# Kernel tuning notes

Hardware: AMD Instinct MI355X
Metric: run time of the kernel (lower is better)

Reference implementation:

```python
import jax, jax.numpy as jnp
import numpy as np

B, K, D, H = 4, 2048, 768, 12
HD = D // H
NEG = -1e30  # stands in for -inf in the additive mask


def setup_inputs() -> dict:
    key = jax.random.key(0)
    ks = jax.random.split(key, 11)
    s = 1.0 / np.sqrt(D)
    inp = {
        "x": jax.random.normal(ks[0], (B, K, D), jnp.float32),
        "is_context": jax.random.randint(ks[1], (B, K), 0, 2) > 0,
        "Wq": jax.random.normal(ks[2], (D, D), jnp.float32) * s,
        "bq": jax.random.normal(ks[3], (D,), jnp.float32) * 0.01,
        "Wk": jax.random.normal(ks[4], (D, D), jnp.float32) * s,
        "bk": jax.random.normal(ks[5], (D,), jnp.float32) * 0.01,
        "Wv": jax.random.normal(ks[6], (D, D), jnp.float32) * s,
        "bv": jax.random.normal(ks[7], (D,), jnp.float32) * 0.01,
        "Wo": jax.random.normal(ks[8], (D, D), jnp.float32) * s,
        "bo": jax.random.normal(ks[9], (D,), jnp.float32) * 0.01,
    }
    return inp


def reference(x, is_context, Wq, bq, Wk, bk, Wv, bv, Wo, bo):
    b, k_len, d = x.shape
    scale = 1.0 / jnp.sqrt(jnp.asarray(HD, x.dtype))
    # torch nn.Linear: y = x @ W.T + b
    q = (x @ Wq.T + bq).reshape(b, k_len, H, HD).transpose(0, 2, 1, 3)  # [B,H,K,hd]
    kk = (x @ Wk.T + bk).reshape(b, k_len, H, HD).transpose(0, 2, 1, 3)
    v = (x @ Wv.T + bv).reshape(b, k_len, H, HD).transpose(0, 2, 1, 3)

    ctx = is_context  # [B,K] bool
    # allowed[b,i,j]: context rows attend only to context cols; target rows attend to all
    allowed = (ctx[:, :, None] & ctx[:, None, :]) | (~ctx)[:, :, None]  # [B,K,K]

    scores = jnp.einsum("bhqd,bhkd->bhqk", q, kk) * scale  # [B,H,K,K]
    scores = jnp.where(allowed[:, None, :, :], scores, NEG)
    attn = jax.nn.softmax(scores, axis=-1)
    out = jnp.einsum("bhqk,bhkd->bhqd", attn, v)  # [B,H,K,hd]
    out = out.transpose(0, 2, 1, 3).reshape(b, k_len, d)
    return out @ Wo.T + bo
```

## Files before the change

### kernel.cpp

```cpp
#include <hip/hip_runtime.h>
#include <hip/hip_bf16.h>

constexpr int BATCH = 4;
constexpr int SEQ   = 2048;
constexpr int DIM   = 768;
constexpr int NH    = 12;
constexpr int HDIM  = 64;

typedef __attribute__((ext_vector_type(8))) short bf16x8;
typedef __attribute__((ext_vector_type(4))) float f32x4;
typedef __attribute__((ext_vector_type(4))) short s16x4;

__device__ inline short f2bf(float f) {
    union { float f; unsigned u; } v; v.f = f;
    unsigned r = (v.u + 0x7fff + ((v.u >> 16) & 1)) >> 16;
    return (short)r;
}

__device__ inline unsigned pack_bf16x2(float a, float b) {
    union { __hip_bfloat162 h; unsigned u; } c;
    c.h = __float22bfloat162_rn(make_float2(a, b));
    return c.u;
}

__device__ inline float fast_exp2(float x) {
#if __has_builtin(__builtin_amdgcn_exp2f)
    return __builtin_amdgcn_exp2f(x);
#else
    return __expf(x * 0.6931471805599453f);
#endif
}

__device__ inline void gld16(const short* g, short* l) {
    __builtin_amdgcn_global_load_lds(
        (const __attribute__((address_space(1))) void*)g,
        (__attribute__((address_space(3))) void*)l, 16, 0, 0);
}

__device__ inline bool ctx_at(const void* p, bool isU8, int idx) {
    return isU8 ? (((const unsigned char*)p)[idx] != 0)
                : (((const int*)p)[idx] != 0);
}

__global__ __launch_bounds__(256) void prep_kernel(
    const float* __restrict__ x,  const float* __restrict__ Wq,
    const float* __restrict__ Wk, const float* __restrict__ Wv,
    const float* __restrict__ Wo,
    short* __restrict__ xb,  short* __restrict__ Wqb,
    short* __restrict__ Wkb, short* __restrict__ Wvb,
    short* __restrict__ Wob,
    const unsigned char* __restrict__ ctxm, int ctxbytes, int* __restrict__ flag) {
    const int blk = blockIdx.x;
    constexpr int XBLK = (BATCH * SEQ * DIM / 4) / 256;
    constexpr int WBLK = (DIM * DIM / 4) / 256;

    if (blk == XBLK + 4 * WBLK) {
        __shared__ int cnt;
        if (threadIdx.x == 0) cnt = 0;
        __syncthreads();
        int local = 0;
        for (int i = threadIdx.x; i < ctxbytes; i += 256)
            if ((i & 3) != 0 && ctxm[i] != 0) local++;
        atomicAdd(&cnt, local);
        __syncthreads();
        if (threadIdx.x == 0) *flag = (cnt > 0) ? 1 : 0;
        return;
    }

    const float* src; short* dst; int i;
    if (blk < XBLK) {
        src = x; dst = xb;
        i = blk * 256 + threadIdx.x;
    } else {
        const int r = blk - XBLK;
        const int w = r / WBLK;
        src = (w == 0) ? Wq : (w == 1) ? Wk : (w == 2) ? Wv : Wo;
        dst = (w == 0) ? Wqb : (w == 1) ? Wkb : (w == 2) ? Wvb : Wob;
        i = (r - w * WBLK) * 256 + threadIdx.x;
    }
    float4 v = ((const float4*)src)[i];
    s16x4 o;
    o.x = f2bf(v.x); o.y = f2bf(v.y); o.z = f2bf(v.z); o.w = f2bf(v.w);
    ((s16x4*)dst)[i] = o;
}

template <bool BF16OUT>
__global__ __launch_bounds__(256) void gemm_mfma(
    const short* __restrict__ A,
    const short* __restrict__ W0, const float* __restrict__ bias0, void* __restrict__ C0,
    const short* __restrict__ W1, const float* __restrict__ bias1, void* __restrict__ C1,
    const short* __restrict__ W2, const float* __restrict__ bias2, void* __restrict__ C2,
    float scale0) {
    constexpr int N  = DIM;
    constexpr int Kd = DIM;

    const short* W; const float* bias; void* C; float scale;
    if (blockIdx.z == 0)      { W = W0; bias = bias0; C = C0; scale = scale0; }
    else if (blockIdx.z == 1) { W = W1; bias = bias1; C = C1; scale = 1.f; }
    else                      { W = W2; bias = bias2; C = C2; scale = 1.f; }

    const int tid  = threadIdx.x;
    const int wave = tid >> 6;
    const int lane = tid & 63;
    const int quad = lane >> 4;
    const int l16  = lane & 15;
    const int wm   = wave & 1;
    const int wn   = wave >> 1;
    const int m0   = blockIdx.y * 128;
    const int n0   = blockIdx.x * 128;

    __shared__ short As[128 * 32];
    __shared__ short Bs[128 * 32];

    const int srow = tid >> 2;
    const int skq  = tid & 3;
    const short* Ag = A + (size_t)(m0 + srow) * Kd + skq * 8;
    const short* Wg = W + (size_t)(n0 + srow) * Kd + skq * 8;
    short* AsP = As + srow * 32 + skq * 8;
    short* BsP = Bs + srow * 32 + skq * 8;

    f32x4 acc[4][4] = {};

    for (int kt = 0; kt < Kd; kt += 32) {
        __syncthreads();
        gld16(Ag + kt,                AsP);
        gld16(Ag + kt + 64 * Kd,      AsP + 64 * 32);
        gld16(Wg + kt,                BsP);
        gld16(Wg + kt + 64 * Kd,      BsP + 64 * 32);
        __syncthreads();

        bf16x8 af[4], bfr[4];
#pragma unroll
        for (int mt = 0; mt < 4; ++mt)
            af[mt] = *(const bf16x8*)&As[(wm * 64 + mt * 16 + l16) * 32 + quad * 8];
#pragma unroll
        for (int nt = 0; nt < 4; ++nt)
            bfr[nt] = *(const bf16x8*)&Bs[(wn * 64 + nt * 16 + l16) * 32 + quad * 8];
#pragma unroll
        for (int mt = 0; mt < 4; ++mt)
#pragma unroll
            for (int nt = 0; nt < 4; ++nt)
                acc[mt][nt] = __builtin_amdgcn_mfma_f32_16x16x32_bf16(
                    af[mt], bfr[nt], acc[mt][nt], 0, 0, 0);
    }

    float bv[4];
#pragma unroll
    for (int nt = 0; nt < 4; ++nt) bv[nt] = bias[n0 + wn * 64 + nt * 16 + l16];

#pragma unroll
    for (int mt = 0; mt < 4; ++mt)
#pragma unroll
        for (int nt = 0; nt < 4; ++nt)
#pragma unroll
            for (int reg = 0; reg < 4; ++reg) {
                const int m = m0 + wm * 64 + mt * 16 + quad * 4 + reg;
                const int n = n0 + wn * 64 + nt * 16 + l16;
                const float v = (acc[mt][nt][reg] + bv[nt]) * scale;
                if (BF16OUT) ((short*)C)[(size_t)m * N + n] = f2bf(v);
                else         ((float*)C)[(size_t)m * N + n] = v;
            }
}

__global__ __launch_bounds__(256) void vtrans_kernel(
    const short* __restrict__ Vb, short* __restrict__ Vtg) {
    const int b  = blockIdx.z;
    const int h  = blockIdx.y;
    const int k0 = blockIdx.x * 64;
    const int pw = threadIdx.x & 15;
    const int d0 = (threadIdx.x >> 4) * 4;

    const int ks = pw >> 3;
    const int w  = pw & 7;
    const int q  = w >> 1;
    const int kbase = ks * 32 + ((w & 1) ? (16 + (q ^ 2) * 4) : (q * 4));

    s16x4 vr[4];
#pragma unroll
    for (int g = 0; g < 4; ++g)
        vr[g] = *(const s16x4*)(Vb + (size_t)(b * SEQ + k0 + kbase + g) * DIM
                                + h * HDIM + d0);
#pragma unroll
    for (int i = 0; i < 4; ++i) {
        s16x4 o = {vr[0][i], vr[1][i], vr[2][i], vr[3][i]};
        *(s16x4*)(Vtg + (size_t)((b * NH + h) * HDIM + d0 + i) * SEQ + k0 + 4 * pw) = o;
    }
}

__global__ __launch_bounds__(256, 3) void attn_mfma8(
    const short* __restrict__ Qb, const short* __restrict__ Kb,
    const short* __restrict__ Vtg, const void* __restrict__ ctxp,
    const int* __restrict__ flagp, short* __restrict__ Ob) {
    const int swz  = (blockIdx.x & 7) * 96 + (blockIdx.x >> 3);
    const int qc   = swz & 15;
    const int h    = (swz >> 4) % NH;
    const int b    = swz / (16 * NH);
    const int q0   = qc * 128;
    const int tid  = threadIdx.x;
    const int wave = tid >> 6;
    const int lane = tid & 63;
    const int quad = lane >> 4;
    const int l16  = lane & 15;
    const bool isU8 = (*flagp != 0);

    __shared__ short Ks[3][64 * 64];
    __shared__ short Vs[3][64 * 64];

    const short* Kg = Kb + (size_t)b * SEQ * DIM + h * HDIM;
    const short* Vg = Vtg + (size_t)(b * NH + h) * HDIM * SEQ;

    const int r0 = tid >> 3;
    const int j0 = (tid & 7) ^ (r0 & 7);
    const int sw = l16 & 7;

    bf16x8 qf[2][2];
#pragma unroll
    for (int rg = 0; rg < 2; ++rg) {
        const short* qp = Qb + (size_t)(b * SEQ + q0 + wave * 32 + rg * 16 + l16) * DIM
                        + h * HDIM + quad * 8;
        qf[rg][0] = *(const bf16x8*)qp;
        qf[rg][1] = *(const bf16x8*)(qp + 32);
    }

    unsigned nmb[2];
#pragma unroll
    for (int rg = 0; rg < 2; ++rg)
        nmb[rg] = ctx_at(ctxp, isU8,
            b * SEQ + q0 + wave * 32 + rg * 16 + l16) ? 0u : 0xFFFFFFFFu;

    constexpr int NT = SEQ / 64;
    unsigned kbits = 0;
    for (int t = 0; t < NT; ++t)
        kbits |= (ctx_at(ctxp, isU8, b * SEQ + t * 64 + lane) ? 1u : 0u) << t;

    bf16x8 ones;
#pragma unroll
    for (int i = 0; i < 8; ++i) ones[i] = (short)0x3F80;

    f32x4 accl[2] = {};
    f32x4 acc[2][4] = {};

    auto stage = [&](int t) {
        short* KD = Ks[t % 3];
        short* VD = Vs[t % 3];
        const int kn = t * 64;
        gld16(Kg + (size_t)(kn + r0) * DIM + j0 * 8,      KD + tid * 8);
        gld16(Kg + (size_t)(kn + r0 + 32) * DIM + j0 * 8, KD + (tid + 256) * 8);
        gld16(Vg + (size_t)r0 * SEQ + kn + j0 * 8,        VD + tid * 8);
        gld16(Vg + (size_t)(r0 + 32) * SEQ + kn + j0 * 8, VD + (tid + 256) * 8);
    };

    stage(0);
    stage(1);

    for (int t = 0; t < NT; ++t) {
        const short* BK = Ks[t % 3];
        const short* BV = Vs[t % 3];

        __builtin_amdgcn_s_barrier();
        __builtin_amdgcn_sched_barrier(0);
        if (t + 2 < NT) stage(t + 2);

        if (t < NT - 2)       asm volatile("s_waitcnt vmcnt(8)" ::: "memory");
        else if (t == NT - 2) asm volatile("s_waitcnt vmcnt(4)" ::: "memory");
        else                  asm volatile("s_waitcnt vmcnt(0)" ::: "memory");
        __builtin_amdgcn_sched_barrier(0);
        __builtin_amdgcn_s_barrier();
        __builtin_amdgcn_sched_barrier(0);

        const unsigned long long kmask = __ballot((kbits >> t) & 1u);

        f32x4 s4[4][2] = {};
        __builtin_amdgcn_s_setprio(1);
#pragma unroll
        for (int ks = 0; ks < 2; ++ks) {
            bf16x8 kf[4];
#pragma unroll
            for (int g = 0; g < 4; ++g)
                kf[g] = *(const bf16x8*)
                    &BK[(g * 16 + l16) * 64 + (((ks * 4 + quad) ^ sw)) * 8];
#pragma unroll
            for (int g = 0; g < 4; ++g) {
                s4[g][0] = __builtin_amdgcn_mfma_f32_16x16x32_bf16(kf[g], qf[0][ks], s4[g][0], 0, 0, 0);
                s4[g][1] = __builtin_amdgcn_mfma_f32_16x16x32_bf16(kf[g], qf[1][ks], s4[g][1], 0, 0, 0);
            }
        }
        __builtin_amdgcn_s_setprio(0);

        unsigned mw[2][4];
#pragma unroll
        for (int ks = 0; ks < 2; ++ks)
#pragma unroll
            for (int w = 0; w < 4; ++w) {
                const int base = 32 * ks + ((w >> 1) & 1) * 16 + quad * 4 + (w & 1) * 2;
                const unsigned two = (unsigned)(kmask >> base) & 3u;
                mw[ks][w] = ((two & 1u) ? 0x0000FFFFu : 0u) |
                            ((two & 2u) ? 0xFFFF0000u : 0u);
            }

        bf16x8 pa[2][2];
#pragma unroll
        for (int rg = 0; rg < 2; ++rg) {
            const unsigned nm = nmb[rg];
#pragma unroll
            for (int ks = 0; ks < 2; ++ks) {
                const int g0 = 2 * ks, g1 = 2 * ks + 1;
                const float e0 = fast_exp2(s4[g0][rg][0]);
                const float e1 = fast_exp2(s4[g0][rg][1]);
                const float e2 = fast_exp2(s4[g0][rg][2]);
                const float e3 = fast_exp2(s4[g0][rg][3]);
                const float e4 = fast_exp2(s4[g1][rg][0]);
                const float e5 = fast_exp2(s4[g1][rg][1]);
                const float e6 = fast_exp2(s4[g1][rg][2]);
                const float e7 = fast_exp2(s4[g1][rg][3]);
                const unsigned wA0 = pack_bf16x2(e0, e1) & (nm | mw[ks][0]);
                const unsigned wA1 = pack_bf16x2(e2, e3) & (nm | mw[ks][1]);
                const unsigned wB0 = pack_bf16x2(e4, e5) & (nm | mw[ks][2]);
                const unsigned wB1 = pack_bf16x2(e6, e7) & (nm | mw[ks][3]);
                const unsigned pB0 = (unsigned)__shfl((int)wB0, lane ^ 32);
                const unsigned pB1 = (unsigned)__shfl((int)wB1, lane ^ 32);
                union { bf16x8 v; unsigned u[4]; } tb;
                tb.u[0] = wA0; tb.u[1] = wA1; tb.u[2] = pB0; tb.u[3] = pB1;
                pa[rg][ks] = tb.v;
            }
        }

        __builtin_amdgcn_s_setprio(1);
#pragma unroll
        for (int ks = 0; ks < 2; ++ks) {
            accl[0] = __builtin_amdgcn_mfma_f32_16x16x32_bf16(pa[0][ks], ones, accl[0], 0, 0, 0);
            accl[1] = __builtin_amdgcn_mfma_f32_16x16x32_bf16(pa[1][ks], ones, accl[1], 0, 0, 0);
#pragma unroll
            for (int dt = 0; dt < 4; ++dt) {
                bf16x8 vf = *(const bf16x8*)
                    &BV[(dt * 16 + l16) * 64 + (((ks * 4 + quad) ^ sw)) * 8];
                acc[0][dt] = __builtin_amdgcn_mfma_f32_16x16x32_bf16(pa[0][ks], vf, acc[0][dt], 0, 0, 0);
                acc[1][dt] = __builtin_amdgcn_mfma_f32_16x16x32_bf16(pa[1][ks], vf, acc[1][dt], 0, 0, 0);
            }
        }
        __builtin_amdgcn_s_setprio(0);
    }

    float inv[2][4];
#pragma unroll
    for (int rg = 0; rg < 2; ++rg)
#pragma unroll
        for (int reg = 0; reg < 4; ++reg)
            inv[rg][reg] = 1.f / accl[rg][reg];

#pragma unroll
    for (int rg = 0; rg < 2; ++rg)
#pragma unroll
        for (int dt = 0; dt < 4; ++dt)
#pragma unroll
            for (int reg = 0; reg < 4; ++reg) {
                const int q = q0 + wave * 32 + rg * 16 + quad * 4 + reg;
                Ob[(size_t)(b * SEQ + q) * DIM + h * HDIM + dt * 16 + l16] =
                    f2bf(acc[rg][dt][reg] * inv[rg][reg]);
            }
}

extern "C" void kernel_launch(void* const* d_in, const int* in_sizes, int n_in,
                              void* d_out, int out_size, void* d_ws, size_t ws_size,
                              hipStream_t stream) {
    const float* x   = (const float*)d_in[0];
    const void*  ctx = d_in[1];
    const float* Wq  = (const float*)d_in[2];
    const float* bq  = (const float*)d_in[3];
    const float* Wk  = (const float*)d_in[4];
    const float* bk  = (const float*)d_in[5];
    const float* Wv  = (const float*)d_in[6];
    const float* bv  = (const float*)d_in[7];
    const float* Wo  = (const float*)d_in[8];
    const float* bo  = (const float*)d_in[9];
    float* out = (float*)d_out;

    char* ws = (char*)d_ws;
    int* flag = (int*)ws;
    const size_t bufbf = (size_t)BATCH * SEQ * DIM * sizeof(short);
    const size_t wbuf  = (size_t)DIM * DIM * sizeof(short);
    short* xb  = (short*)(ws + 256);
    short* Qb  = (short*)(ws + 256 + bufbf);
    short* Kb  = (short*)(ws + 256 + 2 * bufbf);
    short* Vb  = (short*)(ws + 256 + 3 * bufbf);
    short* Ab  = (short*)(ws + 256 + 4 * bufbf);
    short* Vtg = (short*)(ws + 256 + 5 * bufbf);
    short* Wqb = (short*)(ws + 256 + 6 * bufbf);
    short* Wkb = (short*)(ws + 256 + 6 * bufbf + wbuf);
    short* Wvb = (short*)(ws + 256 + 6 * bufbf + 2 * wbuf);
    short* Wob = (short*)(ws + 256 + 6 * bufbf + 3 * wbuf);

    constexpr int XBLK = (BATCH * SEQ * DIM / 4) / 256;
    constexpr int WBLK = (DIM * DIM / 4) / 256;
    prep_kernel<<<XBLK + 4 * WBLK + 1, 256, 0, stream>>>(
        x, Wq, Wk, Wv, Wo, xb, Wqb, Wkb, Wvb, Wob,
        (const unsigned char*)ctx, BATCH * SEQ, flag);

    dim3 gQKV(DIM / 128, (BATCH * SEQ) / 128, 3);
    gemm_mfma<true><<<gQKV, 256, 0, stream>>>(
        xb, Wqb, bq, Qb, Wkb, bk, Kb, Wvb, bv, Vb, 0.125f * 1.4426950408889634f);

    dim3 gVt(SEQ / 64, NH, BATCH);
    vtrans_kernel<<<gVt, 256, 0, stream>>>(Vb, Vtg);

    attn_mfma8<<<dim3(SEQ / 128 * NH * BATCH, 1, 1), 256, 0, stream>>>(
        Qb, Kb, Vtg, ctx, flag, Ab);

    dim3 gOut(DIM / 128, (BATCH * SEQ) / 128, 1);
    gemm_mfma<false><<<gOut, 256, 0, stream>>>(
        Ab, Wob, bo, out, Wob, bo, out, Wob, bo, out, 1.f);
}
```

Measured before the change: 258.7 us.

## Fuse V transpose into QKV GEMM epilogue and software-pipeline QK with softmax-PV

The QKV GEMM now writes V straight into the permuted transposed layout that attention expects, which removes the separate vtrans kernel and its extra round trip through global memory. The attention loop is restructured so the QK^T MFMAs for tile t+1 are issued before the softmax and PV work for tile t, with ping-pong score registers. This lets matrix work overlap the exp and pack ALU work. The cost is more register pressure at 3 blocks per CU, and scattered 8-byte stores in the GEMM epilogue.

New measurement: 262.8 us. No clear change (+1.6%).

```diff
diff --git a/kernel.cpp b/kernel.cpp
--- a/kernel.cpp
+++ b/kernel.cpp
@@ -84,7 +84,7 @@
     ((s16x4*)dst)[i] = o;
 }
 
-template <bool BF16OUT>
+template <bool BF16OUT, bool VT>
 __global__ __launch_bounds__(256) void gemm_mfma(
     const short* __restrict__ A,
     const short* __restrict__ W0, const float* __restrict__ bias0, void* __restrict__ C0,
@@ -148,6 +148,31 @@
 #pragma unroll
     for (int nt = 0; nt < 4; ++nt) bv[nt] = bias[n0 + wn * 64 + nt * 16 + l16];
 
+    if (VT && blockIdx.z == 2) {
+        const int tok0 = m0 + wm * 64;
+        const int bb   = tok0 >> 11;
+        const int tt   = (tok0 & (SEQ - 1)) >> 6;
+        short* Vt = (short*)C;
+#pragma unroll
+        for (int mt = 0; mt < 4; ++mt) {
+            const int p_base = ((mt & 2) << 4) +
+                               ((mt & 1) ? (((quad ^ 2) << 3) + 4) : (quad << 3));
+#pragma unroll
+            for (int nt = 0; nt < 4; ++nt) {
+                const int n    = n0 + wn * 64 + nt * 16 + l16;
+                const int hh   = n >> 6;
+                const int dcol = n & 63;
+                s16x4 o;
+#pragma unroll
+                for (int reg = 0; reg < 4; ++reg)
+                    o[reg] = f2bf(acc[mt][nt][reg] + bv[nt]);
+                *(s16x4*)(Vt + ((size_t)((bb * NH + hh) * HDIM + dcol)) * SEQ
+                          + tt * 64 + p_base) = o;
+            }
+        }
+        return;
+    }
+
 #pragma unroll
     for (int mt = 0; mt < 4; ++mt)
 #pragma unroll
@@ -162,32 +187,7 @@
             }
 }
 
-__global__ __launch_bounds__(256) void vtrans_kernel(
-    const short* __restrict__ Vb, short* __restrict__ Vtg) {
-    const int b  = blockIdx.z;
-    const int h  = blockIdx.y;
-    const int k0 = blockIdx.x * 64;
-    const int pw = threadIdx.x & 15;
-    const int d0 = (threadIdx.x >> 4) * 4;
-
-    const int ks = pw >> 3;
-    const int w  = pw & 7;
-    const int q  = w >> 1;
-    const int kbase = ks * 32 + ((w & 1) ? (16 + (q ^ 2) * 4) : (q * 4));
-
-    s16x4 vr[4];
-#pragma unroll
-    for (int g = 0; g < 4; ++g)
-        vr[g] = *(const s16x4*)(Vb + (size_t)(b * SEQ + k0 + kbase + g) * DIM
-                                + h * HDIM + d0);
-#pragma unroll
-    for (int i = 0; i < 4; ++i) {
-        s16x4 o = {vr[0][i], vr[1][i], vr[2][i], vr[3][i]};
-        *(s16x4*)(Vtg + (size_t)((b * NH + h) * HDIM + d0 + i) * SEQ + k0 + 4 * pw) = o;
-    }
-}
-
-__global__ __launch_bounds__(256, 3) void attn_mfma8(
+__global__ __launch_bounds__(256, 3) void attn_mfma9(
     const short* __restrict__ Qb, const short* __restrict__ Kb,
     const short* __restrict__ Vtg, const void* __restrict__ ctxp,
     const int* __restrict__ flagp, short* __restrict__ Ob) {
@@ -230,6 +230,7 @@
 
     constexpr int NT = SEQ / 64;
     unsigned kbits = 0;
+#pragma unroll
     for (int t = 0; t < NT; ++t)
         kbits |= (ctx_at(ctxp, isU8, b * SEQ + t * 64 + lane) ? 1u : 0u) << t;
 
@@ -250,27 +251,9 @@
         gld16(Vg + (size_t)(r0 + 32) * SEQ + kn + j0 * 8, VD + (tid + 256) * 8);
     };
 
-    stage(0);
-    stage(1);
-
-    for (int t = 0; t < NT; ++t) {
-        const short* BK = Ks[t % 3];
-        const short* BV = Vs[t % 3];
-
-        __builtin_amdgcn_s_barrier();
-        __builtin_amdgcn_sched_barrier(0);
-        if (t + 2 < NT) stage(t + 2);
-
-        if (t < NT - 2)       asm volatile("s_waitcnt vmcnt(8)" ::: "memory");
-        else if (t == NT - 2) asm volatile("s_waitcnt vmcnt(4)" ::: "memory");
-        else                  asm volatile("s_waitcnt vmcnt(0)" ::: "memory");
-        __builtin_amdgcn_sched_barrier(0);
-        __builtin_amdgcn_s_barrier();
-        __builtin_amdgcn_sched_barrier(0);
-
-        const unsigned long long kmask = __ballot((kbits >> t) & 1u);
-
-        f32x4 s4[4][2] = {};
+    auto qk = [&](const short* BK, f32x4 (&sd)[4][2]) {
+#pragma unroll
+        for (int g = 0; g < 4; ++g) { sd[g][0] = (f32x4){}; sd[g][1] = (f32x4){}; }
         __builtin_amdgcn_s_setprio(1);
 #pragma unroll
         for (int ks = 0; ks < 2; ++ks) {
@@ -281,12 +264,15 @@
                     &BK[(g * 16 + l16) * 64 + (((ks * 4 + quad) ^ sw)) * 8];
 #pragma unroll
             for (int g = 0; g < 4; ++g) {
-                s4[g][0] = __builtin_amdgcn_mfma_f32_16x16x32_bf16(kf[g], qf[0][ks], s4[g][0], 0, 0, 0);
-                s4[g][1] = __builtin_amdgcn_mfma_f32_16x16x32_bf16(kf[g], qf[1][ks], s4[g][1], 0, 0, 0);
+                sd[g][0] = __builtin_amdgcn_mfma_f32_16x16x32_bf16(kf[g], qf[0][ks], sd[g][0], 0, 0, 0);
+                sd[g][1] = __builtin_amdgcn_mfma_f32_16x16x32_bf16(kf[g], qf[1][ks], sd[g][1], 0, 0, 0);
             }
         }
         __builtin_amdgcn_s_setprio(0);
-
+    };
+
+    auto sm_pv = [&](f32x4 (&sp)[4][2], int t, const short* BV) {
+        const unsigned long long kmask = __ballot((kbits >> t) & 1u);
         unsigned mw[2][4];
 #pragma unroll
         for (int ks = 0; ks < 2; ++ks)
@@ -305,14 +291,14 @@
 #pragma unroll
             for (int ks = 0; ks < 2; ++ks) {
                 const int g0 = 2 * ks, g1 = 2 * ks + 1;
-                const float e0 = fast_exp2(s4[g0][rg][0]);
-                const float e1 = fast_exp2(s4[g0][rg][1]);
-                const float e2 = fast_exp2(s4[g0][rg][2]);
-                const float e3 = fast_exp2(s4[g0][rg][3]);
-                const float e4 = fast_exp2(s4[g1][rg][0]);
-                const float e5 = fast_exp2(s4[g1][rg][1]);
-                const float e6 = fast_exp2(s4[g1][rg][2]);
-                const float e7 = fast_exp2(s4[g1][rg][3]);
+                const float e0 = fast_exp2(sp[g0][rg][0]);
+                const float e1 = fast_exp2(sp[g0][rg][1]);
+                const float e2 = fast_exp2(sp[g0][rg][2]);
+                const float e3 = fast_exp2(sp[g0][rg][3]);
+                const float e4 = fast_exp2(sp[g1][rg][0]);
+                const float e5 = fast_exp2(sp[g1][rg][1]);
+                const float e6 = fast_exp2(sp[g1][rg][2]);
+                const float e7 = fast_exp2(sp[g1][rg][3]);
                 const unsigned wA0 = pack_bf16x2(e0, e1) & (nm | mw[ks][0]);
                 const unsigned wA1 = pack_bf16x2(e2, e3) & (nm | mw[ks][1]);
                 const unsigned wB0 = pack_bf16x2(e4, e5) & (nm | mw[ks][2]);
@@ -339,6 +325,34 @@
             }
         }
         __builtin_amdgcn_s_setprio(0);
+    };
+
+    f32x4 sA[4][2], sB[4][2];
+
+    stage(0);
+    stage(1);
+    asm volatile("s_waitcnt vmcnt(4)" ::: "memory");
+    __builtin_amdgcn_sched_barrier(0);
+    __builtin_amdgcn_s_barrier();
+    __builtin_amdgcn_sched_barrier(0);
+    qk(Ks[0], sA);
+
+    auto body = [&](int t, f32x4 (&prev)[4][2], f32x4 (&next)[4][2]) {
+        __builtin_amdgcn_s_barrier();
+        __builtin_amdgcn_sched_barrier(0);
+        if (t + 2 < NT) stage(t + 2);
+        if (t < NT - 2) { asm volatile("s_waitcnt vmcnt(4)" ::: "memory"); }
+        else            { asm volatile("s_waitcnt vmcnt(0)" ::: "memory"); }
+        __builtin_amdgcn_sched_barrier(0);
+        __builtin_amdgcn_s_barrier();
+        __builtin_amdgcn_sched_barrier(0);
+        if (t + 1 < NT) qk(Ks[(t + 1) % 3], next);
+        sm_pv(prev, t, Vs[t % 3]);
+    };
+
+    for (int t2 = 0; t2 < NT; t2 += 2) {
+        body(t2,     sA, sB);
+        body(t2 + 1, sB, sA);
     }
 
     float inv[2][4];
@@ -382,7 +396,6 @@
     short* xb  = (short*)(ws + 256);
     short* Qb  = (short*)(ws + 256 + bufbf);
     short* Kb  = (short*)(ws + 256 + 2 * bufbf);
-    short* Vb  = (short*)(ws + 256 + 3 * bufbf);
     short* Ab  = (short*)(ws + 256 + 4 * bufbf);
     short* Vtg = (short*)(ws + 256 + 5 * bufbf);
     short* Wqb = (short*)(ws + 256 + 6 * bufbf);
@@ -397,16 +410,13 @@
         (const unsigned char*)ctx, BATCH * SEQ, flag);
 
     dim3 gQKV(DIM / 128, (BATCH * SEQ) / 128, 3);
-    gemm_mfma<true><<<gQKV, 256, 0, stream>>>(
-        xb, Wqb, bq, Qb, Wkb, bk, Kb, Wvb, bv, Vb, 0.125f * 1.4426950408889634f);
-
-    dim3 gVt(SEQ / 64, NH, BATCH);
-    vtrans_kernel<<<gVt, 256, 0, stream>>>(Vb, Vtg);
-
-    attn_mfma8<<<dim3(SEQ / 128 * NH * BATCH, 1, 1), 256, 0, stream>>>(
+    gemm_mfma<true, true><<<gQKV, 256, 0, stream>>>(
+        xb, Wqb, bq, Qb, Wkb, bk, Kb, Wvb, bv, Vtg, 0.125f * 1.4426950408889634f);
+
+    attn_mfma9<<<dim3(SEQ / 128 * NH * BATCH, 1, 1), 256, 0, stream>>>(
         Qb, Kb, Vtg, ctx, flag, Ab);
 
     dim3 gOut(DIM / 128, (BATCH * SEQ) / 128, 1);
-    gemm_mfma<false><<<gOut, 256, 0, stream>>>(
+    gemm_mfma<false, false><<<gOut, 256, 0, stream>>>(
         Ab, Wob, bo, out, Wob, bo, out, Wob, bo, out, 1.f);
 }
```
